# Kernel optimization log

Hardware: AMD Instinct MI355X
Metric: run time of the kernel (lower is better)

The kernel has to match this reference:

```python
import jax, jax.numpy as jnp
import numpy as np

THETA = 10000.0


def rope_apply(x, pos, theta=THETA):
    # x: [..., S, d] with d even; rotates interleaved pairs (2k, 2k+1),
    # matching the block-diag 2x2 rotation matmul in the torch RoPE.
    d = x.shape[-1]
    half = d // 2
    inv_freq = 1.0 / (theta ** (2.0 * jnp.arange(half, dtype=jnp.float32) / d))
    ang = pos.astype(jnp.float32)[:, None] * inv_freq[None, :]  # [S, half]
    cos, sin = jnp.cos(ang), jnp.sin(ang)
    xe, xo = x[..., 0::2], x[..., 1::2]
    oe = cos * xe - sin * xo
    oo = sin * xe + cos * xo
    return jnp.stack([oe, oo], axis=-1).reshape(x.shape)


def setup_inputs() -> dict:
    key = jax.random.key(0)
    ks = jax.random.split(key, 5)
    B, S, D = 2, 2048, 1024
    scale = 0.02
    return {
        "x": jax.random.normal(ks[0], (B, S, D), dtype=jnp.float32),
        "token_positions": jnp.arange(S, dtype=jnp.int64 if jax.config.jax_enable_x64 else jnp.int32),
        "wq": jax.random.normal(ks[1], (D, D), dtype=jnp.float32) * scale,
        "wk": jax.random.normal(ks[2], (D, D), dtype=jnp.float32) * scale,
        "wv": jax.random.normal(ks[3], (D, D), dtype=jnp.float32) * scale,
        "wo": jax.random.normal(ks[4], (D, D), dtype=jnp.float32) * scale,
    }


def reference(x, token_positions, wq, wk, wv, wo):
    B, S, D = x.shape
    H = 16
    dk = D // H

    def split_heads(t):  # [B,S,D] -> [B,H,S,dk]
        return t.reshape(B, S, H, dk).swapaxes(1, 2)

    q = split_heads(jnp.einsum('bsd,ed->bse', x, wq))
    k = split_heads(jnp.einsum('bsd,ed->bse', x, wk))
    v = split_heads(jnp.einsum('bsd,ed->bse', x, wv))

    q = rope_apply(q, token_positions)
    k = rope_apply(k, token_positions)

    scores = jnp.einsum('bhqd,bhkd->bhqk', q, k) / jnp.sqrt(jnp.float32(dk))
    causal = jnp.tril(jnp.ones((S, S), dtype=bool))
    scores = jnp.where(causal, scores, -jnp.inf)
    p = jax.nn.softmax(scores, axis=-1)
    o = jnp.einsum('bhqk,bhkd->bhqd', p, v)          # [B,H,S,dk]
    o = o.swapaxes(1, 2).reshape(B, S, D)            # merge heads
    return jnp.einsum('bse,de->bsd', o, wo)          # out proj (wo.T)
```

## Files before the change

### kernel.cpp

```cpp
#include <hip/hip_runtime.h>

typedef unsigned short u16;
typedef __attribute__((ext_vector_type(8))) short short8;
typedef __attribute__((ext_vector_type(4))) float f32x4;

__device__ __forceinline__ u16 f2b(float f) {
  union { float f; unsigned u; } v; v.f = f;
  unsigned u = v.u;
  return (u16)((u + 0x7FFFu + ((u >> 16) & 1u)) >> 16);
}
__device__ __forceinline__ u16 f2b_trunc(float f) {
  union { float f; unsigned u; } v; v.f = f;
  return (u16)(v.u >> 16);
}
__device__ __forceinline__ void glds16(const u16* g, u16* l) {
  __builtin_amdgcn_global_load_lds((const __attribute__((address_space(1))) void*)g,
                                   (__attribute__((address_space(3))) void*)l, 16, 0, 0);
}

__global__ __launch_bounds__(256) void prep_k(const float* __restrict__ x,
                                              const float* __restrict__ wq,
                                              const float* __restrict__ wk,
                                              const float* __restrict__ wv,
                                              const float* __restrict__ wo,
                                              const int* __restrict__ pos,
                                              u16* __restrict__ xb,
                                              u16* __restrict__ wqkvb,
                                              u16* __restrict__ wob,
                                              float* __restrict__ cs) {
  int bx = blockIdx.x, tid = threadIdx.x;
  if (bx < 8192) {
    const float* src; u16* dst; int base;
    if (bx < 4096)      { src = x;  dst = xb;                base = bx; }
    else if (bx < 5120) { src = wq; dst = wqkvb;             base = bx - 4096; }
    else if (bx < 6144) { src = wk; dst = wqkvb + (1 << 20); base = bx - 5120; }
    else if (bx < 7168) { src = wv; dst = wqkvb + (2 << 20); base = bx - 6144; }
    else                { src = wo; dst = wob;               base = bx - 7168; }
    int i4 = base * 1024 + tid * 4;
    const float4 v = *(const float4*)(src + i4);
    uint2 o;
    o.x = (unsigned)f2b(v.x) | ((unsigned)f2b(v.y) << 16);
    o.y = (unsigned)f2b(v.z) | ((unsigned)f2b(v.w) << 16);
    *(uint2*)(dst + i4) = o;
  } else {
    int idx = (bx - 8192) * 256 + tid;
    int i = idx & 31, s = idx >> 5;
    float p = (float)pos[s];
    float inv = expf(-(float)i * (logf(10000.0f) / 32.0f));
    float ang = p * inv;
    cs[idx * 2]     = cosf(ang);
    cs[idx * 2 + 1] = sinf(ang);
  }
}

__global__ __launch_bounds__(128, 3) void gemm_qkv(const u16* __restrict__ A,
                                                   const u16* __restrict__ B,
                                                   const float* __restrict__ cs,
                                                   u16* __restrict__ Qr,
                                                   u16* __restrict__ Kr,
                                                   u16* __restrict__ VTg) {
  const int K = 1024;
  __shared__ u16 As[64 * 64];
  __shared__ u16 Bs[128 * 64];
  const int tid = threadIdx.x;
  const int wv = tid >> 6, lane = tid & 63;
  const int quad = lane >> 4, l16 = lane & 15;
  const int m0 = blockIdx.y * 64, n0 = blockIdx.x * 128;
  const int sw = l16 & 7;

  f32x4 acc[4][4];
  for (int i = 0; i < 4; i++)
    for (int j = 0; j < 4; j++) acc[i][j] = (f32x4){0.f, 0.f, 0.f, 0.f};

  for (int kt = 0; kt < K; kt += 64) {
    __syncthreads();
#pragma unroll
    for (int p = 0; p < 4; p++) {
      int c = p * 128 + tid;
      int row = c >> 3, k8 = (c & 7) ^ (row & 7);
      glds16(A + (size_t)(m0 + row) * K + kt + k8 * 8, As + (size_t)(c & ~63) * 8);
    }
#pragma unroll
    for (int p = 0; p < 8; p++) {
      int c = p * 128 + tid;
      int row = c >> 3, k8 = (c & 7) ^ (row & 7);
      glds16(B + (size_t)(n0 + row) * K + kt + k8 * 8, Bs + (size_t)(c & ~63) * 8);
    }
    __syncthreads();
#pragma unroll
    for (int half = 0; half < 2; half++) {
      short8 af[4], bfr[4];
      const int kc = ((half * 4 + quad) ^ sw) * 8;
#pragma unroll
      for (int i = 0; i < 4; i++)
        af[i] = *(const short8*)(As + (i * 16 + l16) * 64 + kc);
#pragma unroll
      for (int j = 0; j < 4; j++)
        bfr[j] = *(const short8*)(Bs + (wv * 64 + j * 16 + l16) * 64 + kc);
#pragma unroll
      for (int i = 0; i < 4; i++)
#pragma unroll
        for (int j = 0; j < 4; j++)
          acc[i][j] = __builtin_amdgcn_mfma_f32_16x16x32_bf16(af[i], bfr[j], acc[i][j], 0, 0, 0);
    }
  }

  const int region = n0 >> 10;
  const int b = m0 >> 11;
  if (region < 2) {
    u16* dst = region ? Kr : Qr;
    const bool evn = (l16 & 1) == 0;
    for (int i = 0; i < 4; i++)
      for (int j = 0; j < 4; j++) {
        int col = n0 + wv * 64 + j * 16 + l16;
        int cq = col & 1023;
        int h = cq >> 6, d = cq & 63, ifr = (d >> 1) & 31;
        for (int r = 0; r < 4; r++) {
          int s = (m0 & 2047) + i * 16 + quad * 4 + r;
          float v = acc[i][j][r];
          float vp = __shfl_xor(v, 1);
          if (evn) {
            float2 c2 = *(const float2*)(cs + (s * 32 + ifr) * 2);
            float oe = c2.x * v - c2.y * vp;
            float oo = c2.y * v + c2.x * vp;
            unsigned pk = (unsigned)f2b(oe) | ((unsigned)f2b(oo) << 16);
            *(unsigned*)(dst + ((size_t)(b * 16 + h) * 2048 + s) * 64 + d) = pk;
          }
        }
      }
  } else {
    for (int j = 0; j < 4; j++) {
      int col = n0 + wv * 64 + j * 16 + l16;
      int cq = col & 1023;
      int h = cq >> 6, d = cq & 63;
      u16* base = VTg + ((size_t)(b * 16 + h) * 64 + d) * 2048;
      for (int i = 0; i < 4; i++) {
        int s0 = (m0 & 2047) + i * 16 + quad * 4;
        uint2 o;
        o.x = (unsigned)f2b(acc[i][j][0]) | ((unsigned)f2b(acc[i][j][1]) << 16);
        o.y = (unsigned)f2b(acc[i][j][2]) | ((unsigned)f2b(acc[i][j][3]) << 16);
        *(uint2*)(base + s0) = o;
      }
    }
  }
}

__global__ __launch_bounds__(128, 3) void gemm_bt_f32(const u16* __restrict__ A,
                                                      const u16* __restrict__ B,
                                                      float* __restrict__ C,
                                                      int M, int N, int K) {
  __shared__ u16 As[64 * 64];
  __shared__ u16 Bs[128 * 64];
  const int tid = threadIdx.x;
  const int wv = tid >> 6, lane = tid & 63;
  const int quad = lane >> 4, l16 = lane & 15;
  const int m0 = blockIdx.y * 64, n0 = blockIdx.x * 128;
  const int sw = l16 & 7;

  f32x4 acc[4][4];
  for (int i = 0; i < 4; i++)
    for (int j = 0; j < 4; j++) acc[i][j] = (f32x4){0.f, 0.f, 0.f, 0.f};

  for (int kt = 0; kt < K; kt += 64) {
    __syncthreads();
#pragma unroll
    for (int p = 0; p < 4; p++) {
      int c = p * 128 + tid;
      int row = c >> 3, k8 = (c & 7) ^ (row & 7);
      glds16(A + (size_t)(m0 + row) * K + kt + k8 * 8, As + (size_t)(c & ~63) * 8);
    }
#pragma unroll
    for (int p = 0; p < 8; p++) {
      int c = p * 128 + tid;
      int row = c >> 3, k8 = (c & 7) ^ (row & 7);
      glds16(B + (size_t)(n0 + row) * K + kt + k8 * 8, Bs + (size_t)(c & ~63) * 8);
    }
    __syncthreads();
#pragma unroll
    for (int half = 0; half < 2; half++) {
      short8 af[4], bfr[4];
      const int kc = ((half * 4 + quad) ^ sw) * 8;
#pragma unroll
      for (int i = 0; i < 4; i++)
        af[i] = *(const short8*)(As + (i * 16 + l16) * 64 + kc);
#pragma unroll
      for (int j = 0; j < 4; j++)
        bfr[j] = *(const short8*)(Bs + (wv * 64 + j * 16 + l16) * 64 + kc);
#pragma unroll
      for (int i = 0; i < 4; i++)
#pragma unroll
        for (int j = 0; j < 4; j++)
          acc[i][j] = __builtin_amdgcn_mfma_f32_16x16x32_bf16(af[i], bfr[j], acc[i][j], 0, 0, 0);
    }
  }
  for (int i = 0; i < 4; i++)
    for (int j = 0; j < 4; j++) {
      int col = n0 + wv * 64 + j * 16 + l16;
      for (int r = 0; r < 4; r++) {
        int row = m0 + i * 16 + quad * 4 + r;
        C[(size_t)row * N + col] = acc[i][j][r];
      }
    }
}

__global__ __launch_bounds__(256, 6) void attn_k(const u16* __restrict__ Q,
                                                 const u16* __restrict__ K,
                                                 const u16* __restrict__ VT,
                                                 float* __restrict__ Op,
                                                 float* __restrict__ Lp, int S) {
  __shared__ u16 Ks[8 * 512], Vt[64 * 64], Ps[8 * 520];
  const int tid = threadIdx.x;
  const int wv = tid >> 6, lane = tid & 63, quad = lane >> 4, l16 = lane & 15;
  const int bh = blockIdx.y, par = blockIdx.z;
  const u16* Qg = Q + (size_t)bh * S * 64;
  const u16* Kg = K + (size_t)bh * S * 64;
  const u16* Vg = VT + (size_t)bh * S * 64;
  const int nqt = S >> 6;
  const float scale2 = 0.125f * 1.44269504f;
  const int rowbase = wv * 16 + quad * 4;
  float* Opb = Op + ((size_t)par * 32 + bh) * S * 64;
  float* Lpb = Lp + ((size_t)par * 32 + bh) * S;

  const int vrow_off = lane >> 3;
  const int vchunk = (lane & 7) ^ (lane >> 3);

  for (int t = 0; t < 2; t++) {
    const int qt = t ? (nqt - 1 - (int)blockIdx.x) : (int)blockIdx.x;
    const int q0 = qt * 64;
    const u16* qrow = Qg + (size_t)(q0 + wv * 16 + l16) * 64;
    short8 qa0 = *(const short8*)(qrow + quad * 8);
    short8 qa1 = *(const short8*)(qrow + 32 + quad * 8);

    f32x4 oacc[4];
    for (int j = 0; j < 4; j++) oacc[j] = (f32x4){0.f, 0.f, 0.f, 0.f};
    float l_r[4] = {0.f, 0.f, 0.f, 0.f};

    for (int kt = par; kt <= qt; kt += 2) {
      const int k0 = kt * 64;
      __syncthreads();
      for (int p = wv; p < 8; p += 4) {
        glds16(Kg + (size_t)(k0 + lane) * 64 + p * 8, Ks + p * 512);
        glds16(Vg + (size_t)(p * 8 + vrow_off) * S + k0 + vchunk * 8, Vt + p * 512);
      }
      __syncthreads();

      const bool diag = (kt == qt);
#pragma unroll
      for (int nt = 0; nt < 4; nt++) {
        f32x4 s4 = (f32x4){0.f, 0.f, 0.f, 0.f};
        short8 b0 = *(const short8*)(Ks + quad * 512 + (nt * 16 + l16) * 8);
        short8 b1 = *(const short8*)(Ks + (4 + quad) * 512 + (nt * 16 + l16) * 8);
        s4 = __builtin_amdgcn_mfma_f32_16x16x32_bf16(qa0, b0, s4, 0, 0, 0);
        s4 = __builtin_amdgcn_mfma_f32_16x16x32_bf16(qa1, b1, s4, 0, 0, 0);
        int col = nt * 16 + l16;
        int cp = col >> 3, co = col & 7;
#pragma unroll
        for (int r = 0; r < 4; r++) {
          float v = s4[r] * scale2;
          v = fminf(v, 86.f);
          if (diag && col > rowbase + r) v = -1e30f;
          float p = exp2f(v);
          l_r[r] += p;
          int row = rowbase + r;
          int A = (cp + 2 * (row >> 3)) & 7;
          Ps[A * 520 + row * 8 + co] = f2b_trunc(p);
        }
      }
      {
        int mr = wv * 16 + l16;
        int A0 = (quad + 2 * (mr >> 3)) & 7;
        short8 pa0 = *(const short8*)(Ps + A0 * 520 + mr * 8);
        short8 pa1 = *(const short8*)(Ps + ((A0 + 4) & 7) * 520 + mr * 8);
        int sl0 = quad ^ (l16 & 7);
#pragma unroll
        for (int nt = 0; nt < 4; nt++) {
          int d = nt * 16 + l16;
          short8 vb0 = *(const short8*)(Vt + d * 64 + sl0 * 8);
          short8 vb1 = *(const short8*)(Vt + d * 64 + (sl0 ^ 4) * 8);
          oacc[nt] = __builtin_amdgcn_mfma_f32_16x16x32_bf16(pa0, vb0, oacc[nt], 0, 0, 0);
          oacc[nt] = __builtin_amdgcn_mfma_f32_16x16x32_bf16(pa1, vb1, oacc[nt], 0, 0, 0);
        }
      }
    }
#pragma unroll
    for (int r = 0; r < 4; r++) {
      l_r[r] += __shfl_xor(l_r[r], 1);
      l_r[r] += __shfl_xor(l_r[r], 2);
      l_r[r] += __shfl_xor(l_r[r], 4);
      l_r[r] += __shfl_xor(l_r[r], 8);
    }
    if (l16 == 0)
#pragma unroll
      for (int r = 0; r < 4; r++) Lpb[q0 + rowbase + r] = l_r[r];
#pragma unroll
    for (int nt = 0; nt < 4; nt++) {
      int col = nt * 16 + l16;
#pragma unroll
      for (int r = 0; r < 4; r++)
        Opb[(size_t)(q0 + rowbase + r) * 64 + col] = oacc[nt][r];
    }
  }
}

__global__ __launch_bounds__(256) void combine_k(const float* __restrict__ Op,
                                                 const float* __restrict__ Lp,
                                                 u16* __restrict__ O, int S) {
  int idx = blockIdx.x * 256 + threadIdx.x;
  int d4 = idx & 15, s = (idx >> 4) & 2047, bh = idx >> 15;
  size_t po = (((size_t)bh * S) + s) * 64 + d4 * 4;
  size_t pstride = (size_t)32 * S * 64;
  float4 a = *(const float4*)(Op + po);
  float4 c = *(const float4*)(Op + pstride + po);
  float l = Lp[(size_t)bh * S + s] + Lp[(size_t)32 * S + (size_t)bh * S + s];
  float rl = 1.f / l;
  int b = bh >> 4, h = bh & 15;
  size_t oo = ((size_t)(b * S + s) * 16 + h) * 64 + d4 * 4;
  uint2 o;
  o.x = (unsigned)f2b((a.x + c.x) * rl) | ((unsigned)f2b((a.y + c.y) * rl) << 16);
  o.y = (unsigned)f2b((a.z + c.z) * rl) | ((unsigned)f2b((a.w + c.w) * rl) << 16);
  *(uint2*)(O + oo) = o;
}

extern "C" void kernel_launch(void* const* d_in, const int* in_sizes, int n_in,
                              void* d_out, int out_size, void* d_ws, size_t ws_size,
                              hipStream_t stream) {
  const float* x  = (const float*)d_in[0];
  const int*   tp = (const int*)d_in[1];
  const float* wq = (const float*)d_in[2];
  const float* wk = (const float*)d_in[3];
  const float* wvp = (const float*)d_in[4];
  const float* wo = (const float*)d_in[5];
  float* out = (float*)d_out;

  const int S = 2048, D = 1024;
  const int BS = 2 * S;

  char* ws = (char*)d_ws;
  u16*   xb    = (u16*)(ws);
  u16*   wqkvb = (u16*)(ws + ((size_t)8 << 20));
  u16*   wob   = (u16*)(ws + ((size_t)14 << 20));
  float* cs    = (float*)(ws + ((size_t)16 << 20));
  u16*   qr    = (u16*)(ws + ((size_t)17 << 20));
  u16*   kr    = (u16*)(ws + ((size_t)25 << 20));
  u16*   vtg   = (u16*)(ws + ((size_t)33 << 20));
  float* lpart = (float*)(ws + ((size_t)41 << 20));
  u16*   ob    = (u16*)(ws + ((size_t)42 << 20));
  float* opart = (float*)(ws + ((size_t)50 << 20));

  prep_k<<<8448, 256, 0, stream>>>(x, wq, wk, wvp, wo, tp, xb, wqkvb, wob, cs);

  dim3 g1(3 * D / 128, BS / 64);
  gemm_qkv<<<g1, 128, 0, stream>>>(xb, wqkvb, cs, qr, kr, vtg);

  dim3 ga(S / 128, 32, 2);
  attn_k<<<ga, 256, 0, stream>>>(qr, kr, vtg, opart, lpart, S);

  combine_k<<<(32 * S * 16) / 256, 256, 0, stream>>>(opart, lpart, ob, S);

  dim3 g2(D / 128, BS / 64);
  gemm_bt_f32<<<g2, 128, 0, stream>>>(ob, wob, out, BS, D, D);
}
```

Measured before the change: 210.5 us.

## Drop split-K attention and combine kernel; one block per query tile

Attention work is now split so each block handles a single 64-row query tile over all its key tiles, instead of two interleaved key-parity partitions processing a pair of tiles. Normalization and bf16 packing move into the attention kernel's epilogue, which removes the fp32 partial output and L buffers and the separate combine kernel launch. The causal mask branch is hoisted so non-diagonal tiles skip the per-element compare. The cost is load imbalance, since block work now varies with query tile index (mitigated by a snake ordering over blockIdx.y), and less parallelism per block chain.

```diff
diff --git a/kernel.cpp b/kernel.cpp
--- a/kernel.cpp
+++ b/kernel.cpp
@@ -206,119 +206,113 @@
 __global__ __launch_bounds__(256, 6) void attn_k(const u16* __restrict__ Q,
                                                  const u16* __restrict__ K,
                                                  const u16* __restrict__ VT,
-                                                 float* __restrict__ Op,
-                                                 float* __restrict__ Lp, int S) {
+                                                 u16* __restrict__ O, int S) {
   __shared__ u16 Ks[8 * 512], Vt[64 * 64], Ps[8 * 520];
   const int tid = threadIdx.x;
   const int wv = tid >> 6, lane = tid & 63, quad = lane >> 4, l16 = lane & 15;
-  const int bh = blockIdx.y, par = blockIdx.z;
+  const int bh = blockIdx.x;
+  const int yy = blockIdx.y, k4 = yy >> 3, g = yy & 7;
+  const int qt = (k4 & 1) ? (k4 * 8 + 7 - g) : (k4 * 8 + g);
+  const int q0 = qt * 64;
   const u16* Qg = Q + (size_t)bh * S * 64;
   const u16* Kg = K + (size_t)bh * S * 64;
   const u16* Vg = VT + (size_t)bh * S * 64;
-  const int nqt = S >> 6;
   const float scale2 = 0.125f * 1.44269504f;
   const int rowbase = wv * 16 + quad * 4;
-  float* Opb = Op + ((size_t)par * 32 + bh) * S * 64;
-  float* Lpb = Lp + ((size_t)par * 32 + bh) * S;
 
   const int vrow_off = lane >> 3;
   const int vchunk = (lane & 7) ^ (lane >> 3);
 
-  for (int t = 0; t < 2; t++) {
-    const int qt = t ? (nqt - 1 - (int)blockIdx.x) : (int)blockIdx.x;
-    const int q0 = qt * 64;
-    const u16* qrow = Qg + (size_t)(q0 + wv * 16 + l16) * 64;
-    short8 qa0 = *(const short8*)(qrow + quad * 8);
-    short8 qa1 = *(const short8*)(qrow + 32 + quad * 8);
-
-    f32x4 oacc[4];
-    for (int j = 0; j < 4; j++) oacc[j] = (f32x4){0.f, 0.f, 0.f, 0.f};
-    float l_r[4] = {0.f, 0.f, 0.f, 0.f};
-
-    for (int kt = par; kt <= qt; kt += 2) {
-      const int k0 = kt * 64;
-      __syncthreads();
-      for (int p = wv; p < 8; p += 4) {
-        glds16(Kg + (size_t)(k0 + lane) * 64 + p * 8, Ks + p * 512);
-        glds16(Vg + (size_t)(p * 8 + vrow_off) * S + k0 + vchunk * 8, Vt + p * 512);
-      }
-      __syncthreads();
-
-      const bool diag = (kt == qt);
-#pragma unroll
-      for (int nt = 0; nt < 4; nt++) {
-        f32x4 s4 = (f32x4){0.f, 0.f, 0.f, 0.f};
-        short8 b0 = *(const short8*)(Ks + quad * 512 + (nt * 16 + l16) * 8);
-        short8 b1 = *(const short8*)(Ks + (4 + quad) * 512 + (nt * 16 + l16) * 8);
-        s4 = __builtin_amdgcn_mfma_f32_16x16x32_bf16(qa0, b0, s4, 0, 0, 0);
-        s4 = __builtin_amdgcn_mfma_f32_16x16x32_bf16(qa1, b1, s4, 0, 0, 0);
-        int col = nt * 16 + l16;
-        int cp = col >> 3, co = col & 7;
+  const u16* qrow = Qg + (size_t)(q0 + wv * 16 + l16) * 64;
+  short8 qa0 = *(const short8*)(qrow + quad * 8);
+  short8 qa1 = *(const short8*)(qrow + 32 + quad * 8);
+
+  f32x4 oacc[4];
+  for (int j = 0; j < 4; j++) oacc[j] = (f32x4){0.f, 0.f, 0.f, 0.f};
+  float l_r[4] = {0.f, 0.f, 0.f, 0.f};
+
+  for (int kt = 0; kt <= qt; kt++) {
+    const int k0 = kt * 64;
+    __syncthreads();
+    for (int p = wv; p < 8; p += 4) {
+      glds16(Kg + (size_t)(k0 + lane) * 64 + p * 8, Ks + p * 512);
+      glds16(Vg + (size_t)(p * 8 + vrow_off) * S + k0 + vchunk * 8, Vt + p * 512);
+    }
+    __syncthreads();
+
+    const bool diag = (kt == qt);
+#pragma unroll
+    for (int nt = 0; nt < 4; nt++) {
+      f32x4 s4 = (f32x4){0.f, 0.f, 0.f, 0.f};
+      short8 b0 = *(const short8*)(Ks + quad * 512 + (nt * 16 + l16) * 8);
+      short8 b1 = *(const short8*)(Ks + (4 + quad) * 512 + (nt * 16 + l16) * 8);
+      s4 = __builtin_amdgcn_mfma_f32_16x16x32_bf16(qa0, b0, s4, 0, 0, 0);
+      s4 = __builtin_amdgcn_mfma_f32_16x16x32_bf16(qa1, b1, s4, 0, 0, 0);
+      int col = nt * 16 + l16;
+      int cp = col >> 3, co = col & 7;
+      if (!diag) {
 #pragma unroll
         for (int r = 0; r < 4; r++) {
-          float v = s4[r] * scale2;
-          v = fminf(v, 86.f);
-          if (diag && col > rowbase + r) v = -1e30f;
+          float v = fminf(s4[r] * scale2, 86.f);
           float p = exp2f(v);
           l_r[r] += p;
           int row = rowbase + r;
           int A = (cp + 2 * (row >> 3)) & 7;
           Ps[A * 520 + row * 8 + co] = f2b_trunc(p);
         }
-      }
-      {
-        int mr = wv * 16 + l16;
-        int A0 = (quad + 2 * (mr >> 3)) & 7;
-        short8 pa0 = *(const short8*)(Ps + A0 * 520 + mr * 8);
-        short8 pa1 = *(const short8*)(Ps + ((A0 + 4) & 7) * 520 + mr * 8);
-        int sl0 = quad ^ (l16 & 7);
-#pragma unroll
-        for (int nt = 0; nt < 4; nt++) {
-          int d = nt * 16 + l16;
-          short8 vb0 = *(const short8*)(Vt + d * 64 + sl0 * 8);
-          short8 vb1 = *(const short8*)(Vt + d * 64 + (sl0 ^ 4) * 8);
-          oacc[nt] = __builtin_amdgcn_mfma_f32_16x16x32_bf16(pa0, vb0, oacc[nt], 0, 0, 0);
-          oacc[nt] = __builtin_amdgcn_mfma_f32_16x16x32_bf16(pa1, vb1, oacc[nt], 0, 0, 0);
+      } else {
+#pragma unroll
+        for (int r = 0; r < 4; r++) {
+          float v = fminf(s4[r] * scale2, 86.f);
+          if (col > rowbase + r) v = -1e30f;
+          float p = exp2f(v);
+          l_r[r] += p;
+          int row = rowbase + r;
+          int A = (cp + 2 * (row >> 3)) & 7;
+          Ps[A * 520 + row * 8 + co] = f2b_trunc(p);
         }
       }
     }
+    {
+      int mr = wv * 16 + l16;
+      int A0 = (quad + 2 * (mr >> 3)) & 7;
+      short8 pa0 = *(const short8*)(Ps + A0 * 520 + mr * 8);
+      short8 pa1 = *(const short8*)(Ps + ((A0 + 4) & 7) * 520 + mr * 8);
+      int sl0 = quad ^ (l16 & 7);
+#pragma unroll
+      for (int nt = 0; nt < 4; nt++) {
+        int d = nt * 16 + l16;
+        short8 vb0 = *(const short8*)(Vt + d * 64 + sl0 * 8);
+        short8 vb1 = *(const short8*)(Vt + d * 64 + (sl0 ^ 4) * 8);
+        oacc[nt] = __builtin_amdgcn_mfma_f32_16x16x32_bf16(pa0, vb0, oacc[nt], 0, 0, 0);
+        oacc[nt] = __builtin_amdgcn_mfma_f32_16x16x32_bf16(pa1, vb1, oacc[nt], 0, 0, 0);
+      }
+    }
+  }
+#pragma unroll
+  for (int r = 0; r < 4; r++) {
+    l_r[r] += __shfl_xor(l_r[r], 1);
+    l_r[r] += __shfl_xor(l_r[r], 2);
+    l_r[r] += __shfl_xor(l_r[r], 4);
+    l_r[r] += __shfl_xor(l_r[r], 8);
+    l_r[r] = 1.f / l_r[r];
+  }
+  const int b = bh >> 4, h = bh & 15;
+  const bool evn = (l16 & 1) == 0;
+#pragma unroll
+  for (int nt = 0; nt < 4; nt++) {
+    int col = nt * 16 + l16;
 #pragma unroll
     for (int r = 0; r < 4; r++) {
-      l_r[r] += __shfl_xor(l_r[r], 1);
-      l_r[r] += __shfl_xor(l_r[r], 2);
-      l_r[r] += __shfl_xor(l_r[r], 4);
-      l_r[r] += __shfl_xor(l_r[r], 8);
-    }
-    if (l16 == 0)
-#pragma unroll
-      for (int r = 0; r < 4; r++) Lpb[q0 + rowbase + r] = l_r[r];
-#pragma unroll
-    for (int nt = 0; nt < 4; nt++) {
-      int col = nt * 16 + l16;
-#pragma unroll
-      for (int r = 0; r < 4; r++)
-        Opb[(size_t)(q0 + rowbase + r) * 64 + col] = oacc[nt][r];
-    }
-  }
-}
-
-__global__ __launch_bounds__(256) void combine_k(const float* __restrict__ Op,
-                                                 const float* __restrict__ Lp,
-                                                 u16* __restrict__ O, int S) {
-  int idx = blockIdx.x * 256 + threadIdx.x;
-  int d4 = idx & 15, s = (idx >> 4) & 2047, bh = idx >> 15;
-  size_t po = (((size_t)bh * S) + s) * 64 + d4 * 4;
-  size_t pstride = (size_t)32 * S * 64;
-  float4 a = *(const float4*)(Op + po);
-  float4 c = *(const float4*)(Op + pstride + po);
-  float l = Lp[(size_t)bh * S + s] + Lp[(size_t)32 * S + (size_t)bh * S + s];
-  float rl = 1.f / l;
-  int b = bh >> 4, h = bh & 15;
-  size_t oo = ((size_t)(b * S + s) * 16 + h) * 64 + d4 * 4;
-  uint2 o;
-  o.x = (unsigned)f2b((a.x + c.x) * rl) | ((unsigned)f2b((a.y + c.y) * rl) << 16);
-  o.y = (unsigned)f2b((a.z + c.z) * rl) | ((unsigned)f2b((a.w + c.w) * rl) << 16);
-  *(uint2*)(O + oo) = o;
+      float v = oacc[nt][r] * l_r[r];
+      float vp = __shfl_xor(v, 1);
+      if (evn) {
+        int s = q0 + rowbase + r;
+        unsigned pk = (unsigned)f2b(v) | ((unsigned)f2b(vp) << 16);
+        *(unsigned*)(O + ((size_t)(b * S + s) * 16 + h) * 64 + col) = pk;
+      }
+    }
+  }
 }
 
 extern "C" void kernel_launch(void* const* d_in, const int* in_sizes, int n_in,
@@ -343,19 +337,15 @@
   u16*   qr    = (u16*)(ws + ((size_t)17 << 20));
   u16*   kr    = (u16*)(ws + ((size_t)25 << 20));
   u16*   vtg   = (u16*)(ws + ((size_t)33 << 20));
-  float* lpart = (float*)(ws + ((size_t)41 << 20));
   u16*   ob    = (u16*)(ws + ((size_t)42 << 20));
-  float* opart = (float*)(ws + ((size_t)50 << 20));
 
   prep_k<<<8448, 256, 0, stream>>>(x, wq, wk, wvp, wo, tp, xb, wqkvb, wob, cs);
 
   dim3 g1(3 * D / 128, BS / 64);
   gemm_qkv<<<g1, 128, 0, stream>>>(xb, wqkvb, cs, qr, kr, vtg);
 
-  dim3 ga(S / 128, 32, 2);
-  attn_k<<<ga, 256, 0, stream>>>(qr, kr, vtg, opart, lpart, S);
-
-  combine_k<<<(32 * S * 16) / 256, 256, 0, stream>>>(opart, lpart, ob, S);
+  dim3 ga(32, 32);
+  attn_k<<<ga, 256, 0, stream>>>(qr, kr, vtg, ob, S);
 
   dim3 g2(D / 128, BS / 64);
   gemm_bt_f32<<<g2, 128, 0, stream>>>(ob, wob, out, BS, D, D);
```

Measured after the change: 205.1 us. -2.6%, faster.
